# Kernel tuning notes

Hardware: AMD Instinct MI355X
Metric: run time of the kernel (lower is better)

Reference implementation:

```python
import jax, jax.numpy as jnp
import numpy as np

B, S, D, H = 4, 2048, 1024, 16
DH = D // H  # 64


def setup_inputs() -> dict:
    key = jax.random.key(0)
    ks = jax.random.split(key, 8)
    sc = 1.0 / np.sqrt(D)
    return {
        "hidden_states": jax.random.normal(ks[0], (B, S, D), jnp.float32),
        "attention_mask": jnp.zeros((B, 1, 1, S), jnp.float32),
        "Wq": jax.random.normal(ks[1], (D, D), jnp.float32) * sc,
        "bq": jnp.zeros((D,), jnp.float32),
        "Wk": jax.random.normal(ks[2], (D, D), jnp.float32) * sc,
        "bk": jnp.zeros((D,), jnp.float32),
        "Wv": jax.random.normal(ks[3], (D, D), jnp.float32) * sc,
        "bv": jnp.zeros((D,), jnp.float32),
    }


def _heads(x):
    # [B,S,D] -> [B,H,S,DH]
    b, s, _ = x.shape
    return x.reshape(b, s, H, DH).transpose(0, 2, 1, 3)


def reference(hidden_states, attention_mask, Wq, bq, Wk, bk, Wv, bv):
    q = _heads(hidden_states @ Wq + bq)
    k = _heads(hidden_states @ Wk + bk)
    v = _heads(hidden_states @ Wv + bv)
    scores = jnp.einsum('bhqd,bhkd->bhqk', q, k) / jnp.sqrt(jnp.float32(DH))
    scores = scores + attention_mask  # additive mask, broadcast
    probs = jax.nn.softmax(scores, axis=-1)  # dropout is identity in eval
    out = jnp.einsum('bhqk,bhkd->bhqd', probs, v)
    b, h, s, dh = out.shape
    return out.transpose(0, 2, 1, 3).reshape(b, s, h * dh)
```

## Files before the change

kernel.cpp:

```cpp
#include <hip/hip_runtime.h>
#include <hip/hip_bf16.h>
#include <cstdint>

typedef _Float16 f16;
typedef f16 f16x8 __attribute__((ext_vector_type(8)));
typedef f16 f16x4 __attribute__((ext_vector_type(4)));
typedef float f32x4 __attribute__((ext_vector_type(4)));

#define MFMA16(a, b, c) __builtin_amdgcn_mfma_f32_16x16x32_f16((a), (b), (c), 0, 0, 0)

constexpr int Bc = 4, Sc = 2048, Dc = 1024, Hc = 16, DHc = 64;

typedef __attribute__((address_space(1))) const uint32_t gbl_u32;
typedef __attribute__((address_space(3))) uint32_t lds_u32;
__device__ __forceinline__ void gld_lds16(const void* g, void* l) {
  __builtin_amdgcn_global_load_lds((gbl_u32*)g, (lds_u32*)l, 16, 0, 0);
}

__global__ __launch_bounds__(256) void cast_w_kernel(
    const float* __restrict__ Wq, const float* __restrict__ Wk,
    const float* __restrict__ Wv, f16* __restrict__ Wt) {
  __shared__ __align__(16) f16 T[64][66];
  const int z = blockIdx.z;
  const float* W = (z == 0) ? Wq : (z == 1) ? Wk : Wv;
  const int n0 = blockIdx.x * 64, k0 = blockIdx.y * 64;
  const int t = threadIdx.x;
#pragma unroll
  for (int p = 0; p < 4; p++) {
    int idx = t + p * 256;
    int r = idx >> 4, c = idx & 15;
    float4 v = *(const float4*)(W + (size_t)(k0 + r) * Dc + n0 + c * 4);
    T[r][c * 4 + 0] = (f16)v.x;
    T[r][c * 4 + 1] = (f16)v.y;
    T[r][c * 4 + 2] = (f16)v.z;
    T[r][c * 4 + 3] = (f16)v.w;
  }
  __syncthreads();
#pragma unroll
  for (int p = 0; p < 2; p++) {
    int idx = t + p * 256;
    int n = idx >> 3, c = idx & 7;
    f16x8 tmp;
#pragma unroll
    for (int j = 0; j < 8; j++) tmp[j] = T[c * 8 + j][n];
    *(f16x8*)(Wt + ((size_t)z * Dc + n0 + n) * Dc + k0 + c * 8) = tmp;
  }
}

__global__ __launch_bounds__(256) void cast_x_kernel(const float* __restrict__ X,
                                                     f16* __restrict__ X16) {
  size_t i = ((size_t)blockIdx.x * 256 + threadIdx.x) * 8;
  float4 a = *(const float4*)(X + i);
  float4 b = *(const float4*)(X + i + 4);
  f16x8 h;
  h[0] = (f16)a.x; h[1] = (f16)a.y; h[2] = (f16)a.z; h[3] = (f16)a.w;
  h[4] = (f16)b.x; h[5] = (f16)b.y; h[6] = (f16)b.z; h[7] = (f16)b.w;
  *(f16x8*)(X16 + i) = h;
}

__global__ __launch_bounds__(256) void qkv_gemm_kernel(
    const f16* __restrict__ X16, const f16* __restrict__ Wt,
    const float* __restrict__ bq, const float* __restrict__ bk,
    const float* __restrict__ bv, f16* __restrict__ Qo, f16* __restrict__ Ko,
    f16* __restrict__ Vo) {
  const int z = blockIdx.z;
  const f16* W = Wt + (size_t)z * Dc * Dc;
  const float* bias = (z == 0) ? bq : (z == 1) ? bk : bv;

  const int n0 = blockIdx.x * 128, m0 = blockIdx.y * 128;
  __shared__ __align__(16) f16 Xs[128 * 32];
  __shared__ __align__(16) f16 Ws[128 * 32];

  const int t = threadIdx.x;
  const int wave = t >> 6, lane = t & 63;
  const int l16 = lane & 15, quad = lane >> 4;
  const int wm = (wave >> 1) * 64, wn = (wave & 1) * 64;

  f32x4 acc[4][4];
#pragma unroll
  for (int i = 0; i < 4; i++)
#pragma unroll
    for (int j = 0; j < 4; j++) acc[i][j] = (f32x4){0.f, 0.f, 0.f, 0.f};

  for (int k0 = 0; k0 < Dc; k0 += 32) {
#pragma unroll
    for (int p = 0; p < 2; p++) {
      int cb = p * 256 + wave * 64;
      int chunk = cb + lane;
      int row = chunk >> 2, c8 = (chunk & 3) * 8;
      gld_lds16(X16 + (size_t)(m0 + row) * Dc + k0 + c8, (f16*)Xs + (size_t)cb * 8);
      gld_lds16(W + (size_t)(n0 + row) * Dc + k0 + c8, (f16*)Ws + (size_t)cb * 8);
    }
    __syncthreads();

    f16x8 aF[4], bF[4];
#pragma unroll
    for (int mt = 0; mt < 4; mt++)
      aF[mt] = *(const f16x8*)(&Xs[(wm + mt * 16 + l16) * 32 + quad * 8]);
#pragma unroll
    for (int nt = 0; nt < 4; nt++)
      bF[nt] = *(const f16x8*)(&Ws[(wn + nt * 16 + l16) * 32 + quad * 8]);
#pragma unroll
    for (int mt = 0; mt < 4; mt++)
#pragma unroll
      for (int nt = 0; nt < 4; nt++)
        acc[mt][nt] = MFMA16(aF[mt], bF[nt], acc[mt][nt]);
    __syncthreads();
  }

#pragma unroll
  for (int nt = 0; nt < 4; nt++) {
    int col = n0 + wn + nt * 16 + l16;
    float bval = bias[col];
    int h = col >> 6, d = col & 63;
    if (z == 2) {
#pragma unroll
      for (int mt = 0; mt < 4; mt++) {
        int m = m0 + wm + mt * 16 + quad * 4;
        int b = m >> 11, sbase = m & 2047;
        f16x4 pk;
#pragma unroll
        for (int r = 0; r < 4; r++) pk[r] = (f16)(acc[mt][nt][r] + bval);
        *(f16x4*)(Vo + (((size_t)(b * Hc + h)) * DHc + d) * Sc + sbase) = pk;
      }
    } else {
      const float sc = (z == 0) ? 0.18033688011112042f : 1.0f;
      f16* O = (z == 0) ? Qo : Ko;
#pragma unroll
      for (int mt = 0; mt < 4; mt++) {
#pragma unroll
        for (int r = 0; r < 4; r++) {
          int m = m0 + wm + mt * 16 + quad * 4 + r;
          int b = m >> 11, s = m & 2047;
          O[(((size_t)(b * Hc + h)) * Sc + s) * DHc + d] =
              (f16)((acc[mt][nt][r] + bval) * sc);
        }
      }
    }
  }
}

__global__ __launch_bounds__(256) void flash_kernel(
    const f16* __restrict__ Q, const f16* __restrict__ K,
    const f16* __restrict__ Vt, const float* __restrict__ mask,
    float* __restrict__ out) {
  const int bh = blockIdx.y;
  const int b = bh >> 4, h = bh & 15;
  const int t = threadIdx.x;
  const int wave = t >> 6, lane = t & 63;
  const int l16 = lane & 15, quad = lane >> 4;
  const int qbase = blockIdx.x * 128 + wave * 32;

  __shared__ __align__(16) f16 Ks[2][4096];
  __shared__ __align__(16) f16 Vs[2][4096];

  const f16* Kb = K + (size_t)bh * Sc * DHc;
  const f16* Vb = Vt + (size_t)bh * DHc * Sc;

  const int qsw8 = (quad ^ ((l16 >> 1) & 3)) * 8;

  const f16* kp[2];
  const f16* vp[2];
  int ldsOff[2];
#pragma unroll
  for (int p = 0; p < 2; p++) {
    int cb = p * 256 + wave * 64;
    int i = cb + lane;
    int half = i >> 8, row = (i >> 2) & 63, q8 = i & 3;
    int q8g = q8 ^ ((row >> 1) & 3);
    int g = (row & 32) | ((row & 12) << 1) | ((row & 16) >> 2) | (row & 3);
    kp[p] = Kb + (size_t)g * DHc + half * 32 + q8g * 8;
    vp[p] = Vb + (size_t)row * Sc + half * 32 + q8g * 8;
    ldsOff[p] = cb * 8;
  }
  auto stage = [&](int buf) {
#pragma unroll
    for (int p = 0; p < 2; p++) {
      gld_lds16(kp[p], (f16*)Ks + buf * 4096 + ldsOff[p]);
      gld_lds16(vp[p], (f16*)Vs + buf * 4096 + ldsOff[p]);
      kp[p] += 64 * DHc;
      vp[p] += 64;
    }
  };

  const float* mp = mask + (size_t)b * Sc + quad * 8;

  f16x8 qa[2][2];
#pragma unroll
  for (int mt = 0; mt < 2; mt++) {
    const f16* qb = Q + ((size_t)bh * Sc + qbase + mt * 16 + l16) * DHc;
    qa[mt][0] = *(const f16x8*)(qb + quad * 8);
    qa[mt][1] = *(const f16x8*)(qb + 32 + quad * 8);
  }

  f16x8 ones;
#pragma unroll
  for (int j = 0; j < 8; j++) ones[j] = (f16)1.0f;

  stage(0);
  __syncthreads();

  f32x4 lacc[2];
  f32x4 o[2][4];
#pragma unroll
  for (int mt = 0; mt < 2; mt++) {
    lacc[mt] = (f32x4){0.f, 0.f, 0.f, 0.f};
#pragma unroll
    for (int dt = 0; dt < 4; dt++) o[mt][dt] = (f32x4){0.f, 0.f, 0.f, 0.f};
  }

  constexpr float L2E = 1.44269504088896340736f;

  for (int c = 0; c < 32; c++) {
    const int buf = c & 1;
    float4 mv[4];
    mv[0] = *(const float4*)(mp + 0);
    mv[1] = *(const float4*)(mp + 4);
    mv[2] = *(const float4*)(mp + 32);
    mv[3] = *(const float4*)(mp + 36);
    mp += 64;
    if (c < 31) stage(buf ^ 1);

    f32x4 minit[4];
#pragma unroll
    for (int nt = 0; nt < 4; nt++)
      minit[nt] = (f32x4){mv[nt].x * L2E, mv[nt].y * L2E, mv[nt].z * L2E,
                          mv[nt].w * L2E};

    f16x8 ka[4][2];
#pragma unroll
    for (int nt = 0; nt < 4; nt++) {
      int rb = (nt * 16 + l16) * 32 + qsw8;
      ka[nt][0] = *(const f16x8*)(&Ks[buf][rb]);
      ka[nt][1] = *(const f16x8*)(&Ks[buf][2048 + rb]);
    }

    f32x4 s0[4], s1[4];
#pragma unroll
    for (int nt = 0; nt < 4; nt++) {
      f32x4 a = minit[nt];
      a = MFMA16(ka[nt][0], qa[0][0], a);
      a = MFMA16(ka[nt][1], qa[0][1], a);
      s0[nt] = a;
      f32x4 a2 = minit[nt];
      a2 = MFMA16(ka[nt][0], qa[1][0], a2);
      a2 = MFMA16(ka[nt][1], qa[1][1], a2);
      s1[nt] = a2;
    }

    f16x8 pa[2][2];
#pragma unroll
    for (int blk = 0; blk < 2; blk++) {
      f16x8 p0, p1;
#pragma unroll
      for (int half = 0; half < 2; half++) {
        int nt = blk * 2 + half;
#pragma unroll
        for (int r = 0; r < 4; r++) {
          p0[half * 4 + r] = (f16)__builtin_amdgcn_exp2f(s0[nt][r]);
          p1[half * 4 + r] = (f16)__builtin_amdgcn_exp2f(s1[nt][r]);
        }
      }
      pa[0][blk] = p0;
      pa[1][blk] = p1;
    }

    lacc[0] = MFMA16(pa[0][0], ones, lacc[0]);
    lacc[0] = MFMA16(pa[0][1], ones, lacc[0]);
    lacc[1] = MFMA16(pa[1][0], ones, lacc[1]);
    lacc[1] = MFMA16(pa[1][1], ones, lacc[1]);

#pragma unroll
    for (int dt = 0; dt < 4; dt++) {
      int rb = (dt * 16 + l16) * 32 + qsw8;
      f16x8 v0 = *(const f16x8*)(&Vs[buf][rb]);
      f16x8 v1 = *(const f16x8*)(&Vs[buf][2048 + rb]);
      o[0][dt] = MFMA16(pa[0][0], v0, o[0][dt]);
      o[0][dt] = MFMA16(pa[0][1], v1, o[0][dt]);
      o[1][dt] = MFMA16(pa[1][0], v0, o[1][dt]);
      o[1][dt] = MFMA16(pa[1][1], v1, o[1][dt]);
    }

    __syncthreads();
  }

#pragma unroll
  for (int mt = 0; mt < 2; mt++) {
    float inv[4];
#pragma unroll
    for (int r = 0; r < 4; r++) inv[r] = 1.0f / lacc[mt][r];
#pragma unroll
    for (int dt = 0; dt < 4; dt++) {
      int col = h * 64 + dt * 16 + l16;
#pragma unroll
      for (int r = 0; r < 4; r++) {
        int row = qbase + mt * 16 + quad * 4 + r;
        out[((size_t)b * Sc + row) * Dc + col] = o[mt][dt][r] * inv[r];
      }
    }
  }
}

extern "C" void kernel_launch(void* const* d_in, const int* in_sizes, int n_in,
                              void* d_out, int out_size, void* d_ws,
                              size_t ws_size, hipStream_t stream) {
  (void)in_sizes; (void)n_in; (void)out_size; (void)ws_size;
  const float* hidden = (const float*)d_in[0];
  const float* mask   = (const float*)d_in[1];
  const float* Wq     = (const float*)d_in[2];
  const float* bq     = (const float*)d_in[3];
  const float* Wk     = (const float*)d_in[4];
  const float* bk     = (const float*)d_in[5];
  const float* Wv     = (const float*)d_in[6];
  const float* bv     = (const float*)d_in[7];
  float* out = (float*)d_out;

  uint8_t* w = (uint8_t*)d_ws;
  f16* Wt   = (f16*)(w);
  f16* X16  = (f16*)(w + (size_t)6 * 1024 * 1024);
  f16* Q16  = (f16*)(w + (size_t)22 * 1024 * 1024);
  f16* K16  = (f16*)(w + (size_t)38 * 1024 * 1024);
  f16* Vt16 = (f16*)(w + (size_t)54 * 1024 * 1024);

  cast_w_kernel<<<dim3(16, 16, 3), 256, 0, stream>>>(Wq, Wk, Wv, Wt);
  cast_x_kernel<<<4096, 256, 0, stream>>>(hidden, X16);
  qkv_gemm_kernel<<<dim3(8, 64, 3), 256, 0, stream>>>(X16, Wt, bq, bk, bv,
                                                      Q16, K16, Vt16);
  flash_kernel<<<dim3(16, 64), 256, 0, stream>>>(Q16, K16, Vt16, mask, out);
}
```

Measured before the change: 283.8 us.

## Remap GEMM and flash blocks to XCDs and stage mask in LDS

Both the QKV GEMM and the flash kernel switch to a 1D grid. Block indices are remapped so that blocks sharing the same X rows (GEMM) or the same batch-head K/V (flash) land on the same XCD and reuse its L2. The flash kernel also preloads the whole mask row, prescaled by log2(e), into LDS once per block instead of reading it from global memory on every chunk. This adds 8KB of LDS per flash block, which could lower occupancy.

```diff
diff --git a/kernel.cpp b/kernel.cpp
--- a/kernel.cpp
+++ b/kernel.cpp
@@ -63,11 +63,16 @@
     const float* __restrict__ bq, const float* __restrict__ bk,
     const float* __restrict__ bv, f16* __restrict__ Qo, f16* __restrict__ Ko,
     f16* __restrict__ Vo) {
-  const int z = blockIdx.z;
-  const f16* W = Wt + (size_t)z * Dc * Dc;
+  const int lin = blockIdx.x;
+  const int xcd = lin & 7, jj = lin >> 3;
+  const int bn = jj >> 3;
+  const int bm = (xcd << 3) | (jj & 7);
+  const int z = bn >> 3;
+  const int n0 = (bn & 7) * 128;
+  const int m0 = bm * 128;
+  const f16* W = Wt + (size_t)bn * 128 * Dc;
   const float* bias = (z == 0) ? bq : (z == 1) ? bk : bv;
 
-  const int n0 = blockIdx.x * 128, m0 = blockIdx.y * 128;
   __shared__ __align__(16) f16 Xs[128 * 32];
   __shared__ __align__(16) f16 Ws[128 * 32];
 
@@ -89,7 +94,7 @@
       int chunk = cb + lane;
       int row = chunk >> 2, c8 = (chunk & 3) * 8;
       gld_lds16(X16 + (size_t)(m0 + row) * Dc + k0 + c8, (f16*)Xs + (size_t)cb * 8);
-      gld_lds16(W + (size_t)(n0 + row) * Dc + k0 + c8, (f16*)Ws + (size_t)cb * 8);
+      gld_lds16(W + (size_t)row * Dc + k0 + c8, (f16*)Ws + (size_t)cb * 8);
     }
     __syncthreads();
 
@@ -144,18 +149,24 @@
     const f16* __restrict__ Q, const f16* __restrict__ K,
     const f16* __restrict__ Vt, const float* __restrict__ mask,
     float* __restrict__ out) {
-  const int bh = blockIdx.y;
+  const int lin = blockIdx.x;
+  const int xcd = lin & 7, jj = lin >> 3;
+  const int bh = (xcd << 3) | (jj & 7);
+  const int qt = jj >> 3;
   const int b = bh >> 4, h = bh & 15;
   const int t = threadIdx.x;
   const int wave = t >> 6, lane = t & 63;
   const int l16 = lane & 15, quad = lane >> 4;
-  const int qbase = blockIdx.x * 128 + wave * 32;
+  const int qbase = qt * 128 + wave * 32;
 
   __shared__ __align__(16) f16 Ks[2][4096];
   __shared__ __align__(16) f16 Vs[2][4096];
+  __shared__ __align__(16) float Ms[2048];
 
   const f16* Kb = K + (size_t)bh * Sc * DHc;
   const f16* Vb = Vt + (size_t)bh * DHc * Sc;
+
+  constexpr float L2E = 1.44269504088896340736f;
 
   const int qsw8 = (quad ^ ((l16 >> 1) & 3)) * 8;
 
@@ -183,8 +194,6 @@
     }
   };
 
-  const float* mp = mask + (size_t)b * Sc + quad * 8;
-
   f16x8 qa[2][2];
 #pragma unroll
   for (int mt = 0; mt < 2; mt++) {
@@ -198,6 +207,15 @@
   for (int j = 0; j < 8; j++) ones[j] = (f16)1.0f;
 
   stage(0);
+  {
+    const float* mrow = mask + (size_t)b * Sc + t * 8;
+    float4 a0 = *(const float4*)(mrow);
+    float4 a1 = *(const float4*)(mrow + 4);
+    f32x4 m0 = (f32x4){a0.x * L2E, a0.y * L2E, a0.z * L2E, a0.w * L2E};
+    f32x4 m1 = (f32x4){a1.x * L2E, a1.y * L2E, a1.z * L2E, a1.w * L2E};
+    *(f32x4*)(&Ms[t * 8]) = m0;
+    *(f32x4*)(&Ms[t * 8 + 4]) = m1;
+  }
   __syncthreads();
 
   f32x4 lacc[2];
@@ -209,23 +227,16 @@
     for (int dt = 0; dt < 4; dt++) o[mt][dt] = (f32x4){0.f, 0.f, 0.f, 0.f};
   }
 
-  constexpr float L2E = 1.44269504088896340736f;
-
   for (int c = 0; c < 32; c++) {
     const int buf = c & 1;
-    float4 mv[4];
-    mv[0] = *(const float4*)(mp + 0);
-    mv[1] = *(const float4*)(mp + 4);
-    mv[2] = *(const float4*)(mp + 32);
-    mv[3] = *(const float4*)(mp + 36);
-    mp += 64;
     if (c < 31) stage(buf ^ 1);
 
+    const int mb = c * 64 + quad * 8;
     f32x4 minit[4];
-#pragma unroll
-    for (int nt = 0; nt < 4; nt++)
-      minit[nt] = (f32x4){mv[nt].x * L2E, mv[nt].y * L2E, mv[nt].z * L2E,
-                          mv[nt].w * L2E};
+    minit[0] = *(const f32x4*)(&Ms[mb + 0]);
+    minit[1] = *(const f32x4*)(&Ms[mb + 4]);
+    minit[2] = *(const f32x4*)(&Ms[mb + 32]);
+    minit[3] = *(const f32x4*)(&Ms[mb + 36]);
 
     f16x8 ka[4][2];
 #pragma unroll
@@ -324,7 +335,7 @@
 
   cast_w_kernel<<<dim3(16, 16, 3), 256, 0, stream>>>(Wq, Wk, Wv, Wt);
   cast_x_kernel<<<4096, 256, 0, stream>>>(hidden, X16);
-  qkv_gemm_kernel<<<dim3(8, 64, 3), 256, 0, stream>>>(X16, Wt, bq, bk, bv,
-                                                      Q16, K16, Vt16);
-  flash_kernel<<<dim3(16, 64), 256, 0, stream>>>(Q16, K16, Vt16, mask, out);
-}
+  qkv_gemm_kernel<<<dim3(1536), 256, 0, stream>>>(X16, Wt, bq, bk, bv,
+                                                  Q16, K16, Vt16);
+  flash_kernel<<<dim3(1024), 256, 0, stream>>>(Q16, K16, Vt16, mask, out);
+}
```

After: 257.3 us. 1.1x faster.
